# Kernel optimization log

Hardware: AMD Instinct MI355X
Metric: run time of the kernel (lower is better)

Reference implementation:

```python
import jax, jax.numpy as jnp
import numpy as np

H = 32        # num query heads
KVH = 8       # num kv heads
HD = 64       # head dim
G = H // KVH  # GQA group size
THETA = 10000.0


def _rope(x, pos):
    # x: [B, h, S, HD], pos: [B, S] int
    inv_freq = 1.0 / (THETA ** (jnp.arange(0, HD, 2, dtype=jnp.float32) / HD))  # [HD/2]
    freqs = pos.astype(jnp.float32)[:, :, None] * inv_freq[None, None, :]        # [B, S, HD/2]
    emb = jnp.concatenate([freqs, freqs], axis=-1)                               # [B, S, HD]
    cos = jnp.cos(emb)[:, None, :, :].astype(x.dtype)                            # [B, 1, S, HD]
    sin = jnp.sin(emb)[:, None, :, :].astype(x.dtype)
    x1, x2 = x[..., : HD // 2], x[..., HD // 2 :]
    rot = jnp.concatenate([-x2, x1], axis=-1)
    return x * cos + rot * sin


def setup_inputs() -> dict:
    key = jax.random.key(0)
    ks = jax.random.split(key, 8)
    B, S, D = 2, 2048, 2048
    s = 0.02
    hidden_states = jax.random.normal(ks[0], (B, S, D), dtype=jnp.float32)
    position_ids = jnp.broadcast_to(jnp.arange(S, dtype=jnp.int32)[None, :], (B, S))
    Wq = jax.random.normal(ks[1], (H * HD, D), dtype=jnp.float32) * s
    bq = jax.random.normal(ks[2], (H * HD,), dtype=jnp.float32) * s
    Wk = jax.random.normal(ks[3], (KVH * HD, D), dtype=jnp.float32) * s
    bk = jax.random.normal(ks[4], (KVH * HD,), dtype=jnp.float32) * s
    Wv = jax.random.normal(ks[5], (KVH * HD, D), dtype=jnp.float32) * s
    bv = jax.random.normal(ks[6], (KVH * HD,), dtype=jnp.float32) * s
    Wo = jax.random.normal(ks[7], (D, H * HD), dtype=jnp.float32) * s
    return dict(hidden_states=hidden_states, position_ids=position_ids,
                Wq=Wq, bq=bq, Wk=Wk, bk=bk, Wv=Wv, bv=bv, Wo=Wo)


def reference(hidden_states, position_ids, Wq, bq, Wk, bk, Wv, bv, Wo):
    B, S, D = hidden_states.shape
    scale = 1.0 / np.sqrt(HD)
    q = hidden_states @ Wq.T + bq  # [B, S, H*HD]
    k = hidden_states @ Wk.T + bk  # [B, S, KVH*HD]
    v = hidden_states @ Wv.T + bv
    q = q.reshape(B, S, H, HD).transpose(0, 2, 1, 3)      # [B, H, S, HD]
    k = k.reshape(B, S, KVH, HD).transpose(0, 2, 1, 3)    # [B, KVH, S, HD]
    v = v.reshape(B, S, KVH, HD).transpose(0, 2, 1, 3)
    q = _rope(q, position_ids)
    k = _rope(k, position_ids)
    # GQA: view q as [B, KVH, G, S, HD]; equivalent math to repeat_kv of k/v
    qg = q.reshape(B, KVH, G, S, HD)
    scores = jnp.einsum('bkgqd,bkld->bkgql', qg, k) * scale  # [B, KVH, G, S, S]
    # causal mask (past_seq_len = 0)
    causal = jnp.tril(jnp.ones((S, S), dtype=bool))
    scores = jnp.where(causal[None, None, None, :, :], scores, jnp.float32(-jnp.inf))
    attn = jax.nn.softmax(scores.astype(jnp.float32), axis=-1).astype(q.dtype)
    out = jnp.einsum('bkgql,bkld->bkgqd', attn, v)            # [B, KVH, G, S, HD]
    out = out.reshape(B, H, S, HD).transpose(0, 2, 1, 3).reshape(B, S, H * HD)
    return out @ Wo.T
```

## Files before the change

kernel.cpp:

```cpp
#include <hip/hip_runtime.h>
#include <hip/hip_bf16.h>

typedef unsigned short u16;
typedef __bf16 bf16x8 __attribute__((ext_vector_type(8)));
typedef float f32x4 __attribute__((ext_vector_type(4)));
typedef float f32x4v __attribute__((ext_vector_type(4)));
typedef unsigned short u16x4 __attribute__((ext_vector_type(4)));

__device__ __forceinline__ u16 f2bf(float f) {
  __bf16 h = (__bf16)f;
  return __builtin_bit_cast(unsigned short, h);
}

__device__ __forceinline__ int permh(int ph) {
  int blk = ph >> 4;
  int pblk = (blk == 1) ? 2 : ((blk == 2) ? 1 : blk);
  return (pblk << 4) | (ph & 15);
}

__device__ __forceinline__ int SW(int r, int c) {
  return (r << 6) + (c ^ ((r & 7) << 3));
}

#define GLOAD_LDS16(gp, lp) __builtin_amdgcn_global_load_lds( \
    (const __attribute__((address_space(1))) unsigned int*)(gp), \
    (__attribute__((address_space(3))) unsigned int*)(lp), 16, 0, 0)

#define BAR() do { asm volatile("" ::: "memory"); __builtin_amdgcn_s_barrier(); asm volatile("" ::: "memory"); } while (0)
#define VMCNT(n) asm volatile("s_waitcnt vmcnt(" #n ")" ::: "memory")
#define SBAR0() __builtin_amdgcn_sched_barrier(0)

__global__ void prep_all(const f32x4v* __restrict__ hs, u16x4* __restrict__ hsb,
                         const f32x4v* __restrict__ wq, const f32x4v* __restrict__ wk,
                         const f32x4v* __restrict__ wv, u16x4* __restrict__ wqkvb,
                         const f32x4v* __restrict__ wo, u16x4* __restrict__ wob,
                         const int* __restrict__ pos, float* __restrict__ cosT,
                         float* __restrict__ sinT, const float* __restrict__ bq,
                         const float* __restrict__ bk, const float* __restrict__ bv,
                         float* __restrict__ bc) {
  int i = blockIdx.x * 256 + threadIdx.x;
  if (i < 2097152) {
    f32x4v v = hs[i];
    u16x4 o; o.x = f2bf(v.x); o.y = f2bf(v.y); o.z = f2bf(v.z); o.w = f2bf(v.w);
    hsb[i] = o;
  } else if (i < 3670016) {
    int j = i - 2097152;
    int row = j >> 9, c4 = j & 511;
    f32x4v v;
    if (row < 2048) {
      int sr = (row & ~63) | permh(row & 63);
      v = wq[(size_t)sr * 512 + c4];
    } else if (row < 2560) {
      int rk = row - 2048;
      int sr = (rk & ~63) | permh(rk & 63);
      v = wk[(size_t)sr * 512 + c4];
    } else {
      v = wv[(size_t)(row - 2560) * 512 + c4];
    }
    u16x4 o; o.x = f2bf(v.x); o.y = f2bf(v.y); o.z = f2bf(v.z); o.w = f2bf(v.w);
    wqkvb[j] = o;
  } else if (i < 4718592) {
    int j = i - 3670016;
    f32x4v v = wo[j];
    u16x4 o; o.x = f2bf(v.x); o.y = f2bf(v.y); o.z = f2bf(v.z); o.w = f2bf(v.w);
    wob[j] = o;
  } else if (i < 4849664) {
    int j = i - 4718592;
    int bs = j >> 5, f = j & 31;
    float inv = exp2f(-(float)f * (13.287712379549449f / 32.f));
    float ang = (float)pos[bs] * inv;
    cosT[j] = cosf(ang);
    sinT[j] = sinf(ang);
  } else if (i < 4852736) {
    int j = i - 4849664;
    float v;
    if (j < 2048) {
      v = bq[(j & ~63) | permh(j & 63)];
    } else if (j < 2560) {
      int jk = j - 2048;
      v = bk[(jk & ~63) | permh(jk & 63)];
    } else {
      v = bv[j - 2560];
    }
    bc[j] = v;
  }
}

#define STAGE_A(kt, hh) { \
    const u16* s_ = aS + (size_t)(hh) * (BM / 2) * K + (size_t)(kt) * 64; \
    u16* d_ = lds + ((kt) & 1) * BUF + (hh) * (BM * 32) + wid * 512; \
    GLOAD_LDS16(s_, d_); \
    if constexpr (BM == 256) GLOAD_LDS16(s_ + (size_t)64 * K, d_ + 4096); \
  }

#define STAGE_B(kt, hh) { \
    const u16* s_ = bS + (size_t)(hh) * 128 * K + (size_t)(kt) * 64; \
    u16* d_ = lds + ((kt) & 1) * BUF + BM * 64 + (hh) * 8192 + wid * 512; \
    GLOAD_LDS16(s_, d_); \
    GLOAD_LDS16(s_ + (size_t)64 * K, d_ + 4096); \
  }

#define LDA8(buf, qm) { \
    const u16* p_ = lds + (buf) * BUF + ((qm) * (BM / 2) + arow) * 64; \
    _Pragma("unroll") \
    for (int mf = 0; mf < MF; ++mf) { \
      af[mf][0] = *(const bf16x8*)(p_ + mf * 1024 + koff0); \
      af[mf][1] = *(const bf16x8*)(p_ + mf * 1024 + koff1); \
    } }

#define LDB8(buf, qn) { \
    const u16* p_ = lds + (buf) * BUF + BM * 64 + ((qn) * 128 + brow) * 64; \
    _Pragma("unroll") \
    for (int nf = 0; nf < 2; ++nf) { \
      bfr[nf][0] = *(const bf16x8*)(p_ + nf * 1024 + koff0); \
      bfr[nf][1] = *(const bf16x8*)(p_ + nf * 1024 + koff1); \
    } }

#define MM8(qm, qn) { \
    __builtin_amdgcn_s_setprio(1); \
    _Pragma("unroll") \
    for (int mf = 0; mf < MF; ++mf) \
      _Pragma("unroll") \
      for (int nf = 0; nf < 2; ++nf) { \
        acc[(qm) * MF + mf][(qn) * 2 + nf] = __builtin_amdgcn_mfma_f32_16x16x32_bf16( \
            af[mf][0], bfr[nf][0], acc[(qm) * MF + mf][(qn) * 2 + nf], 0, 0, 0); \
        acc[(qm) * MF + mf][(qn) * 2 + nf] = __builtin_amdgcn_mfma_f32_16x16x32_bf16( \
            af[mf][1], bfr[nf][1], acc[(qm) * MF + mf][(qn) * 2 + nf], 0, 0, 0); \
      } \
    __builtin_amdgcn_s_setprio(0); }

#define VMCNT_GATE() do { if constexpr (BM == 256) { VMCNT(6); } else { VMCNT(4); } } while (0)

template <int MODE, int BM>
__global__ __launch_bounds__(512, 2) void gemm8(
    const u16* __restrict__ A, const u16* __restrict__ Bw, const int K, const int N,
    u16* __restrict__ qb, u16* __restrict__ kb, u16* __restrict__ vtb,
    const float* __restrict__ biasc, const float* __restrict__ cosT,
    const float* __restrict__ sinT, float* __restrict__ outf) {
  constexpr int MF = BM / 64;
  constexpr int BUF = BM * 64 + 16384;
  __shared__ u16 lds[2 * BUF];
  const int tid = threadIdx.x;
  const int lane = tid & 63, wid = tid >> 6;
  const int wr = wid >> 2, wc = wid & 3;
  const int col = lane & 15, rg = lane >> 4;
  const int tm = blockIdx.x, tn = blockIdx.y;

  const int srow = tid >> 3;
  const int scol = ((tid & 7) ^ (srow & 7)) * 8;
  const u16* aS = A + ((size_t)tm * BM + srow) * K + scol;
  const u16* bS = Bw + ((size_t)tn * 256 + srow) * K + scol;

  const int koff0 = (rg ^ (col & 7)) * 8;
  const int koff1 = ((4 + rg) ^ (col & 7)) * 8;
  const int arow = wr * (BM / 4) + col;
  const int brow = wc * 32 + col;

  f32x4 acc[2 * MF][4];
#pragma unroll
  for (int i = 0; i < 2 * MF; ++i)
#pragma unroll
    for (int j = 0; j < 4; ++j) acc[i][j] = (f32x4){0.f, 0.f, 0.f, 0.f};
  bf16x8 af[MF][2], bfr[2][2];

  const int ITERS = K >> 7;

  STAGE_A(0, 0); STAGE_A(0, 1);
  STAGE_B(0, 0); STAGE_B(0, 1);
  STAGE_A(1, 0); STAGE_B(1, 1); STAGE_A(1, 1);
  VMCNT_GATE();
  BAR();

#pragma unroll 1
  for (int it = 0; it < ITERS; ++it) {
    const int t0 = it * 2;
    const bool more = (it + 1 < ITERS);
    LDA8(0, 0); LDB8(0, 0);
    STAGE_B(t0 + 1, 0);
    MM8(0, 0); SBAR0(); BAR();
    LDB8(0, 1);
    if (more) STAGE_A(t0 + 2, 0);
    MM8(0, 1); SBAR0(); BAR();
    LDA8(0, 1);
    if (more) STAGE_B(t0 + 2, 1);
    MM8(1, 1); SBAR0(); BAR();
    LDB8(0, 0);
    if (more) STAGE_A(t0 + 2, 1);
    MM8(1, 0); SBAR0();
    if (more) { VMCNT_GATE(); } else { VMCNT(0); }
    BAR();
    LDA8(1, 0); LDB8(1, 0);
    if (more) STAGE_B(t0 + 2, 0);
    MM8(0, 0); SBAR0(); BAR();
    LDB8(1, 1);
    if (more) STAGE_A(t0 + 3, 0);
    MM8(0, 1); SBAR0(); BAR();
    LDA8(1, 1);
    if (more) STAGE_B(t0 + 3, 1);
    MM8(1, 1); SBAR0(); BAR();
    LDB8(1, 0);
    if (more) STAGE_A(t0 + 3, 1);
    MM8(1, 0); SBAR0();
    if (more) VMCNT_GATE();
    BAR();
  }

  if constexpr (MODE == 1) {
#pragma unroll
    for (int qm = 0; qm < 2; ++qm)
#pragma unroll
      for (int mf = 0; mf < MF; ++mf) {
        const int mbase = tm * BM + qm * (BM / 2) + wr * (BM / 4) + mf * 16 + rg * 4;
#pragma unroll
        for (int qn = 0; qn < 2; ++qn)
#pragma unroll
          for (int nf = 0; nf < 2; ++nf) {
            const int n = tn * 256 + qn * 128 + wc * 32 + nf * 16 + col;
#pragma unroll
            for (int r = 0; r < 4; ++r)
              outf[(size_t)(mbase + r) * N + n] = acc[qm * MF + mf][qn * 2 + nf][r];
          }
      }
  } else {
    if (tn < 8) {
      const float QS = 0.18033688011112042f;
#pragma unroll
      for (int qm = 0; qm < 2; ++qm)
#pragma unroll
        for (int qn = 0; qn < 2; ++qn) {
          const int h = tn * 4 + qn * 2 + (wc >> 1);
          const int c32 = wc & 1;
          const int n0 = tn * 256 + qn * 128 + wc * 32 + col;
          const float b1 = biasc[n0], b2 = biasc[n0 + 16];
          const int f = c32 * 16 + col;
          const int ph0 = c32 * 32 + col;
#pragma unroll
          for (int mf = 0; mf < MF; ++mf)
#pragma unroll
            for (int r = 0; r < 4; ++r) {
              const int m = tm * 256 + qm * 128 + wr * 64 + mf * 16 + rg * 4 + r;
              const int b = m >> 11, s = m & 2047;
              const size_t base = ((size_t)(b * 32 + h) * 2048 + s) * 64;
              float x1 = acc[qm * MF + mf][qn * 2 + 0][r] + b1;
              float x2 = acc[qm * MF + mf][qn * 2 + 1][r] + b2;
              float c = cosT[m * 32 + f], sn = sinT[m * 32 + f];
              qb[base + ph0]      = f2bf((x1 * c - x2 * sn) * QS);
              qb[base + ph0 + 16] = f2bf((x2 * c + x1 * sn) * QS);
            }
        }
    } else if (tn < 10) {
#pragma unroll
      for (int qm = 0; qm < 2; ++qm)
#pragma unroll
        for (int qn = 0; qn < 2; ++qn) {
          const int hk = (tn - 8) * 4 + qn * 2 + (wc >> 1);
          const int c32 = wc & 1;
          const int n0 = tn * 256 + qn * 128 + wc * 32 + col;
          const float b1 = biasc[n0], b2 = biasc[n0 + 16];
          const int f = c32 * 16 + col;
          const int ph0 = c32 * 32 + col;
#pragma unroll
          for (int mf = 0; mf < MF; ++mf)
#pragma unroll
            for (int r = 0; r < 4; ++r) {
              const int m = tm * 256 + qm * 128 + wr * 64 + mf * 16 + rg * 4 + r;
              const int b = m >> 11, s = m & 2047;
              const size_t base = ((size_t)(b * 8 + hk) * 2048 + s) * 64;
              float x1 = acc[qm * MF + mf][qn * 2 + 0][r] + b1;
              float x2 = acc[qm * MF + mf][qn * 2 + 1][r] + b2;
              float c = cosT[m * 32 + f], sn = sinT[m * 32 + f];
              kb[base + ph0]      = f2bf(x1 * c - x2 * sn);
              kb[base + ph0 + 16] = f2bf(x2 * c + x1 * sn);
            }
        }
    } else {
#pragma unroll
      for (int qm = 0; qm < 2; ++qm)
#pragma unroll
        for (int qn = 0; qn < 2; ++qn)
#pragma unroll
          for (int nf = 0; nf < 2; ++nf) {
            const int n = tn * 256 + qn * 128 + wc * 32 + nf * 16 + col;
            const int hk = (n - 2560) >> 6;
            const int d = (n - 2560) & 63;
            const float bvv = biasc[n];
#pragma unroll
            for (int mf = 0; mf < MF; ++mf)
#pragma unroll
              for (int r = 0; r < 4; ++r) {
                const int m = tm * 256 + qm * 128 + wr * 64 + mf * 16 + rg * 4 + r;
                const int b = m >> 11, s = m & 2047;
                vtb[((size_t)(b * 8 + hk) * 64 + d) * 2048 + s] =
                    f2bf(acc[qm * MF + mf][qn * 2 + nf][r] + bvv);
              }
          }
    }
  }
}

__global__ __launch_bounds__(256, 4) void attn_k(
    const u16* __restrict__ qb, const u16* __restrict__ kb,
    const u16* __restrict__ vtb, u16* __restrict__ attb) {
  __shared__ __align__(16) u16 Kl[3][2048];
  __shared__ __align__(16) u16 Vl[3][2048];
  __shared__ __align__(16) u16 Pl[4096];
  const int tid = threadIdx.x, lane = tid & 63, w = tid >> 6;
  const int col = lane & 15, rg = lane >> 4;

  const int bid = blockIdx.x;
  const int xcd = bid & 7, pos = bid >> 3;
  const int grp = xcd * 8 + (pos >> 4);
  const int s0 = pos & 15;
  const int strip = ((pos >> 5) & 1) ? (15 - s0) : s0;
  const int h = grp & 31, b = grp >> 5;
  const int qb0 = (15 - strip) * 128;
  const int hk = h >> 2;
  const int q0w = qb0 + w * 32;

  const u16* Qp = qb + ((size_t)(b * 32 + h) * 2048 + q0w + col) * 64 + rg * 8;
  bf16x8 qf[2][2];
#pragma unroll
  for (int g = 0; g < 2; ++g)
#pragma unroll
    for (int kf = 0; kf < 2; ++kf)
      qf[g][kf] = *(const bf16x8*)(Qp + g * 16 * 64 + kf * 32);

  f32x4 po[2][4];
  float l_part[2] = {0.f, 0.f};
#pragma unroll
  for (int g = 0; g < 2; ++g)
#pragma unroll
    for (int cf = 0; cf < 4; ++cf) po[g][cf] = (f32x4){0, 0, 0, 0};

  const u16* Kbase = kb + (size_t)(b * 8 + hk) * 2048 * 64;
  const u16* Vbase = vtb + (size_t)(b * 8 + hk) * 64 * 2048;
  const int srow = tid >> 3, c8 = (tid & 7) << 3;
  const int cs = c8 ^ ((srow & 7) << 3);
  const u16* Ksrc = Kbase + (size_t)srow * 64 + cs;
  const u16* Vsrc = Vbase + (size_t)(srow * 2 + (cs >> 5)) * 2048 + (cs & 31);
  char* Kdst0 = (char*)Kl + w * 1024;
  char* Vdst0 = (char*)Vl + w * 1024;

  const int nkv = (qb0 >> 5) + 4;
  const int rowmax = q0w + 31;

  GLOAD_LDS16(Ksrc, Kdst0);
  GLOAD_LDS16(Vsrc, Vdst0);
  GLOAD_LDS16(Ksrc + 2048, Kdst0 + 4096);
  GLOAD_LDS16(Vsrc + 32, Vdst0 + 4096);

  for (int it = 0; it < nkv; ++it) {
    const int kv0 = it * 32;
    const int buf = it % 3;
    if (it + 2 < nkv) {
      const int b2 = (it + 2) % 3;
      GLOAD_LDS16(Ksrc + (size_t)(it + 2) * 2048, Kdst0 + b2 * 4096);
      GLOAD_LDS16(Vsrc + (size_t)(it + 2) * 32, Vdst0 + b2 * 4096);
      VMCNT(4);
    } else if (it + 1 < nkv) {
      VMCNT(2);
    } else {
      VMCNT(0);
    }
    BAR();

    if (kv0 <= rowmax) {
      const u16* Kb = (const u16*)((const char*)Kl + buf * 4096);
      const u16* Vb = (const u16*)((const char*)Vl + buf * 4096);
      const bool diag = (kv0 + 32 > q0w);

#pragma unroll
      for (int cj = 0; cj < 2; ++cj) {
        const int krow = cj * 16 + col;
        bf16x8 k0f = *(const bf16x8*)&Kb[SW(krow, rg * 8)];
        bf16x8 k1f = *(const bf16x8*)&Kb[SW(krow, 32 + rg * 8)];
#pragma unroll
        for (int g = 0; g < 2; ++g) {
          f32x4 t = (f32x4){0, 0, 0, 0};
          t = __builtin_amdgcn_mfma_f32_16x16x32_bf16(k0f, qf[g][0], t, 0, 0, 0);
          t = __builtin_amdgcn_mfma_f32_16x16x32_bf16(k1f, qf[g][1], t, 0, 0, 0);
          const int q = q0w + g * 16 + col;
          if (diag) {
            const int kbase = kv0 + cj * 16 + rg * 4;
#pragma unroll
            for (int r = 0; r < 4; ++r)
              if (kbase + r > q) t[r] = -1e30f;
          }
          float p0 = __builtin_amdgcn_exp2f(t[0]);
          float p1 = __builtin_amdgcn_exp2f(t[1]);
          float p2 = __builtin_amdgcn_exp2f(t[2]);
          float p3 = __builtin_amdgcn_exp2f(t[3]);
          l_part[g] += (p0 + p1) + (p2 + p3);
          unsigned w0, w1;
          asm("v_cvt_pk_bf16_f32 %0, %1, %2" : "=v"(w0) : "v"(p0), "v"(p1));
          asm("v_cvt_pk_bf16_f32 %0, %1, %2" : "=v"(w1) : "v"(p2), "v"(p3));
          const int lq = w * 32 + g * 16 + col;
          const int prow = lq >> 1;
          const int pc = ((lq & 1) * 32 + cj * 16 + rg * 4) ^ ((prow & 7) << 3);
          *(uint2*)&Pl[prow * 64 + pc] = (uint2){w0, w1};
        }
      }

      __builtin_amdgcn_s_setprio(1);
      {
        bf16x8 pfr[2];
#pragma unroll
        for (int g = 0; g < 2; ++g) {
          const int lq = w * 32 + g * 16 + col;
          const int prow = lq >> 1;
          pfr[g] = *(const bf16x8*)&Pl[prow * 64 +
                     (((lq & 1) * 32 + rg * 8) ^ ((prow & 7) << 3))];
        }
#pragma unroll
        for (int cf = 0; cf < 4; ++cf) {
          const int d = cf * 16 + col;
          const int vrow = d >> 1;
          bf16x8 vf = *(const bf16x8*)&Vb[vrow * 64 +
                       (((d & 1) * 32 + rg * 8) ^ ((vrow & 7) << 3))];
          po[0][cf] = __builtin_amdgcn_mfma_f32_16x16x32_bf16(pfr[0], vf, po[0][cf], 0, 0, 0);
          po[1][cf] = __builtin_amdgcn_mfma_f32_16x16x32_bf16(pfr[1], vf, po[1][cf], 0, 0, 0);
        }
      }
      __builtin_amdgcn_s_setprio(0);
    }
    SBAR0();
    BAR();
  }

#pragma unroll
  for (int g = 0; g < 2; ++g) {
    float l = l_part[g];
    l += __shfl_xor(l, 16);
    l += __shfl_xor(l, 32);
    l_part[g] = l;
  }
#pragma unroll
  for (int g = 0; g < 2; ++g)
#pragma unroll
    for (int r = 0; r < 4; ++r) {
      const float lq = __shfl(l_part[g], rg * 4 + r, 16);
      const float inv = 1.f / lq;
      const int qrow = q0w + g * 16 + rg * 4 + r;
      size_t base = ((size_t)b * 2048 + qrow) * 2048 + h * 64;
#pragma unroll
      for (int cf = 0; cf < 4; ++cf)
        attb[base + cf * 16 + col] = f2bf(po[g][cf][r] * inv);
    }
}

extern "C" void kernel_launch(void* const* d_in, const int* in_sizes, int n_in,
                              void* d_out, int out_size, void* d_ws, size_t ws_size,
                              hipStream_t stream) {
  const float* hs = (const float*)d_in[0];
  const int* pos = (const int*)d_in[1];
  const float* Wq = (const float*)d_in[2];
  const float* bq = (const float*)d_in[3];
  const float* Wk = (const float*)d_in[4];
  const float* bk = (const float*)d_in[5];
  const float* Wv = (const float*)d_in[6];
  const float* bv = (const float*)d_in[7];
  const float* Wo = (const float*)d_in[8];
  float* out = (float*)d_out;

  char* ws = (char*)d_ws;
  size_t off = 0;
  u16* hsb = (u16*)(ws + off);   off += (size_t)4096 * 2048 * 2;
  u16* wqkvb = (u16*)(ws + off); off += (size_t)3072 * 2048 * 2;
  u16* wob = (u16*)(ws + off);   off += (size_t)2048 * 2048 * 2;
  float* biasc = (float*)(ws + off); off += 3072 * 4;
  float* cosT = (float*)(ws + off);  off += (size_t)4096 * 32 * 4;
  float* sinT = (float*)(ws + off);  off += (size_t)4096 * 32 * 4;
  u16* qb = (u16*)(ws + off);    off += (size_t)2 * 32 * 2048 * 64 * 2;
  u16* kb = (u16*)(ws + off);    off += (size_t)2 * 8 * 2048 * 64 * 2;
  u16* vtb = (u16*)(ws + off);   off += (size_t)2 * 8 * 64 * 2048 * 2;
  u16* attb = (u16*)(ws + off);  off += (size_t)4096 * 2048 * 2;

  prep_all<<<18956, 256, 0, stream>>>((const f32x4v*)hs, (u16x4*)hsb,
                                      (const f32x4v*)Wq, (const f32x4v*)Wk,
                                      (const f32x4v*)Wv, (u16x4*)wqkvb,
                                      (const f32x4v*)Wo, (u16x4*)wob,
                                      pos, cosT, sinT, bq, bk, bv, biasc);

  gemm8<0, 256><<<dim3(16, 12), 512, 0, stream>>>(hsb, wqkvb, 2048, 3072,
                                                  qb, kb, vtb, biasc, cosT, sinT, nullptr);
  attn_k<<<1024, 256, 0, stream>>>(qb, kb, vtb, attb);
  gemm8<1, 128><<<dim3(32, 8), 512, 0, stream>>>(attb, wob, 2048, 2048,
                                                 nullptr, nullptr, nullptr, nullptr,
                                                 nullptr, nullptr, out);
}
```

Measured before the change: 174.3 us.

## Double-buffer GEMM LDS fragments in registers to prefetch ahead of MFMA

The GEMM main loop now keeps two register sets each for the A and B fragments. The LDS reads for the next MFMA phase are issued before the current phase's MFMAs, so LDS latency overlaps with matrix math. The first fragments are loaded in the prologue and the last phase prefetches the next iteration's data. The vmcnt wait thresholds move to match the reordered staging. The extra fragment registers add VGPR pressure under the 512x2 launch bounds and could cause spills or lower occupancy.

```diff
diff --git a/kernel.cpp b/kernel.cpp
--- a/kernel.cpp
+++ b/kernel.cpp
@@ -100,36 +100,37 @@
     GLOAD_LDS16(s_ + (size_t)64 * K, d_ + 4096); \
   }
 
-#define LDA8(buf, qm) { \
+#define LDA8_TO(dst, buf, qm) { \
     const u16* p_ = lds + (buf) * BUF + ((qm) * (BM / 2) + arow) * 64; \
     _Pragma("unroll") \
     for (int mf = 0; mf < MF; ++mf) { \
-      af[mf][0] = *(const bf16x8*)(p_ + mf * 1024 + koff0); \
-      af[mf][1] = *(const bf16x8*)(p_ + mf * 1024 + koff1); \
+      dst[mf][0] = *(const bf16x8*)(p_ + mf * 1024 + koff0); \
+      dst[mf][1] = *(const bf16x8*)(p_ + mf * 1024 + koff1); \
     } }
 
-#define LDB8(buf, qn) { \
+#define LDB8_TO(dst, buf, qn) { \
     const u16* p_ = lds + (buf) * BUF + BM * 64 + ((qn) * 128 + brow) * 64; \
     _Pragma("unroll") \
     for (int nf = 0; nf < 2; ++nf) { \
-      bfr[nf][0] = *(const bf16x8*)(p_ + nf * 1024 + koff0); \
-      bfr[nf][1] = *(const bf16x8*)(p_ + nf * 1024 + koff1); \
+      dst[nf][0] = *(const bf16x8*)(p_ + nf * 1024 + koff0); \
+      dst[nf][1] = *(const bf16x8*)(p_ + nf * 1024 + koff1); \
     } }
 
-#define MM8(qm, qn) { \
+#define MM8_W(afs, bfs, qm, qn) { \
     __builtin_amdgcn_s_setprio(1); \
     _Pragma("unroll") \
     for (int mf = 0; mf < MF; ++mf) \
       _Pragma("unroll") \
       for (int nf = 0; nf < 2; ++nf) { \
         acc[(qm) * MF + mf][(qn) * 2 + nf] = __builtin_amdgcn_mfma_f32_16x16x32_bf16( \
-            af[mf][0], bfr[nf][0], acc[(qm) * MF + mf][(qn) * 2 + nf], 0, 0, 0); \
+            afs[mf][0], bfs[nf][0], acc[(qm) * MF + mf][(qn) * 2 + nf], 0, 0, 0); \
         acc[(qm) * MF + mf][(qn) * 2 + nf] = __builtin_amdgcn_mfma_f32_16x16x32_bf16( \
-            af[mf][1], bfr[nf][1], acc[(qm) * MF + mf][(qn) * 2 + nf], 0, 0, 0); \
+            afs[mf][1], bfs[nf][1], acc[(qm) * MF + mf][(qn) * 2 + nf], 0, 0, 0); \
       } \
     __builtin_amdgcn_s_setprio(0); }
 
-#define VMCNT_GATE() do { if constexpr (BM == 256) { VMCNT(6); } else { VMCNT(4); } } while (0)
+#define VM_G() do { if constexpr (BM == 256) { VMCNT(4); } else { VMCNT(3); } } while (0)
+#define VM_PRO() do { if constexpr (BM == 256) { VMCNT(6); } else { VMCNT(4); } } while (0)
 
 template <int MODE, int BM>
 __global__ __launch_bounds__(512, 2) void gemm8(
@@ -161,48 +162,51 @@
   for (int i = 0; i < 2 * MF; ++i)
 #pragma unroll
     for (int j = 0; j < 4; ++j) acc[i][j] = (f32x4){0.f, 0.f, 0.f, 0.f};
-  bf16x8 af[MF][2], bfr[2][2];
+  bf16x8 afX[MF][2], afY[MF][2], bfA[2][2], bfB[2][2];
 
   const int ITERS = K >> 7;
 
   STAGE_A(0, 0); STAGE_A(0, 1);
   STAGE_B(0, 0); STAGE_B(0, 1);
   STAGE_A(1, 0); STAGE_B(1, 1); STAGE_A(1, 1);
-  VMCNT_GATE();
+  VM_PRO();
   BAR();
+  LDA8_TO(afX, 0, 0); LDB8_TO(bfA, 0, 0);
 
 #pragma unroll 1
   for (int it = 0; it < ITERS; ++it) {
     const int t0 = it * 2;
     const bool more = (it + 1 < ITERS);
-    LDA8(0, 0); LDB8(0, 0);
     STAGE_B(t0 + 1, 0);
-    MM8(0, 0); SBAR0(); BAR();
-    LDB8(0, 1);
+    LDB8_TO(bfB, 0, 1);
+    SBAR0(); MM8_W(afX, bfA, 0, 0); SBAR0(); BAR();
     if (more) STAGE_A(t0 + 2, 0);
-    MM8(0, 1); SBAR0(); BAR();
-    LDA8(0, 1);
+    LDA8_TO(afY, 0, 1);
+    SBAR0(); MM8_W(afX, bfB, 0, 1); SBAR0(); BAR();
     if (more) STAGE_B(t0 + 2, 1);
-    MM8(1, 1); SBAR0(); BAR();
-    LDB8(0, 0);
+    LDB8_TO(bfA, 0, 0);
+    SBAR0(); MM8_W(afY, bfB, 1, 1); SBAR0();
+    if (more) { VM_G(); } else { VMCNT(0); }
+    BAR();
     if (more) STAGE_A(t0 + 2, 1);
-    MM8(1, 0); SBAR0();
-    if (more) { VMCNT_GATE(); } else { VMCNT(0); }
+    LDA8_TO(afX, 1, 0); LDB8_TO(bfB, 1, 0);
+    SBAR0(); MM8_W(afY, bfA, 1, 0); SBAR0(); BAR();
+    if (more) STAGE_B(t0 + 2, 0);
+    LDB8_TO(bfA, 1, 1);
+    SBAR0(); MM8_W(afX, bfB, 0, 0); SBAR0(); BAR();
+    if (more) STAGE_A(t0 + 3, 0);
+    LDA8_TO(afY, 1, 1);
+    SBAR0(); MM8_W(afX, bfA, 0, 1); SBAR0(); BAR();
+    if (more) STAGE_B(t0 + 3, 1);
+    LDB8_TO(bfB, 1, 0);
+    SBAR0(); MM8_W(afY, bfA, 1, 1); SBAR0();
+    if (more) VM_G();
     BAR();
-    LDA8(1, 0); LDB8(1, 0);
-    if (more) STAGE_B(t0 + 2, 0);
-    MM8(0, 0); SBAR0(); BAR();
-    LDB8(1, 1);
-    if (more) STAGE_A(t0 + 3, 0);
-    MM8(0, 1); SBAR0(); BAR();
-    LDA8(1, 1);
-    if (more) STAGE_B(t0 + 3, 1);
-    MM8(1, 1); SBAR0(); BAR();
-    LDB8(1, 0);
-    if (more) STAGE_A(t0 + 3, 1);
-    MM8(1, 0); SBAR0();
-    if (more) VMCNT_GATE();
-    BAR();
+    if (more) {
+      STAGE_A(t0 + 3, 1);
+      LDA8_TO(afX, 0, 0); LDB8_TO(bfA, 0, 0);
+    }
+    SBAR0(); MM8_W(afY, bfB, 1, 0); SBAR0(); BAR();
   }
 
   if constexpr (MODE == 1) {
```

Measured after the change: 207.9 us. +19.3%, slower.

## Switch attention to 32x32x16 MFMA and keep P in registers via permlane swap

Applied to the files above, without the earlier changes.

The attention kernel now computes each wave's 32x32 score tile with 32x32x16 bf16 MFMAs instead of 16x16x32 tiles. The exp'd probabilities are packed to bf16 and rearranged across lanes with v_permlane32_swap, so they feed the PV MFMA straight from registers. This drops the LDS round-trip for P and its shared buffer, and the row-sum reduction and output store are simplified to match the new layout. The cost is higher register pressure from the 16-wide accumulators, and the cross-lane layout must be exactly right for the result to be correct.

```diff
diff --git a/kernel.cpp b/kernel.cpp
--- a/kernel.cpp
+++ b/kernel.cpp
@@ -4,12 +4,21 @@
 typedef unsigned short u16;
 typedef __bf16 bf16x8 __attribute__((ext_vector_type(8)));
 typedef float f32x4 __attribute__((ext_vector_type(4)));
+typedef float f32x16 __attribute__((ext_vector_type(16)));
 typedef float f32x4v __attribute__((ext_vector_type(4)));
 typedef unsigned short u16x4 __attribute__((ext_vector_type(4)));
+typedef unsigned int u32x4 __attribute__((ext_vector_type(4)));
 
 __device__ __forceinline__ u16 f2bf(float f) {
   __bf16 h = (__bf16)f;
   return __builtin_bit_cast(unsigned short, h);
+}
+
+__device__ __forceinline__ f32x16 z16() {
+  f32x16 z;
+#pragma unroll
+  for (int i = 0; i < 16; ++i) z[i] = 0.f;
+  return z;
 }
 
 __device__ __forceinline__ int permh(int ph) {
@@ -303,9 +312,8 @@
     const u16* __restrict__ vtb, u16* __restrict__ attb) {
   __shared__ __align__(16) u16 Kl[3][2048];
   __shared__ __align__(16) u16 Vl[3][2048];
-  __shared__ __align__(16) u16 Pl[4096];
   const int tid = threadIdx.x, lane = tid & 63, w = tid >> 6;
-  const int col = lane & 15, rg = lane >> 4;
+  const int q32 = lane & 31, hl = lane >> 5, h4 = hl * 4;
 
   const int bid = blockIdx.x;
   const int xcd = bid & 7, pos = bid >> 3;
@@ -317,20 +325,14 @@
   const int hk = h >> 2;
   const int q0w = qb0 + w * 32;
 
-  const u16* Qp = qb + ((size_t)(b * 32 + h) * 2048 + q0w + col) * 64 + rg * 8;
-  bf16x8 qf[2][2];
-#pragma unroll
-  for (int g = 0; g < 2; ++g)
-#pragma unroll
-    for (int kf = 0; kf < 2; ++kf)
-      qf[g][kf] = *(const bf16x8*)(Qp + g * 16 * 64 + kf * 32);
-
-  f32x4 po[2][4];
-  float l_part[2] = {0.f, 0.f};
-#pragma unroll
-  for (int g = 0; g < 2; ++g)
-#pragma unroll
-    for (int cf = 0; cf < 4; ++cf) po[g][cf] = (f32x4){0, 0, 0, 0};
+  const u16* Qp = qb + ((size_t)(b * 32 + h) * 2048 + q0w + q32) * 64 + hl * 8;
+  bf16x8 qf[4];
+#pragma unroll
+  for (int s = 0; s < 4; ++s) qf[s] = *(const bf16x8*)(Qp + s * 16);
+
+  f32x16 po[2];
+  po[0] = z16(); po[1] = z16();
+  float l_part = 0.f;
 
   const u16* Kbase = kb + (size_t)(b * 8 + hk) * 2048 * 64;
   const u16* Vbase = vtb + (size_t)(b * 8 + hk) * 64 * 2048;
@@ -369,57 +371,50 @@
       const u16* Vb = (const u16*)((const char*)Vl + buf * 4096);
       const bool diag = (kv0 + 32 > q0w);
 
-#pragma unroll
-      for (int cj = 0; cj < 2; ++cj) {
-        const int krow = cj * 16 + col;
-        bf16x8 k0f = *(const bf16x8*)&Kb[SW(krow, rg * 8)];
-        bf16x8 k1f = *(const bf16x8*)&Kb[SW(krow, 32 + rg * 8)];
-#pragma unroll
-        for (int g = 0; g < 2; ++g) {
-          f32x4 t = (f32x4){0, 0, 0, 0};
-          t = __builtin_amdgcn_mfma_f32_16x16x32_bf16(k0f, qf[g][0], t, 0, 0, 0);
-          t = __builtin_amdgcn_mfma_f32_16x16x32_bf16(k1f, qf[g][1], t, 0, 0, 0);
-          const int q = q0w + g * 16 + col;
-          if (diag) {
-            const int kbase = kv0 + cj * 16 + rg * 4;
-#pragma unroll
-            for (int r = 0; r < 4; ++r)
-              if (kbase + r > q) t[r] = -1e30f;
-          }
-          float p0 = __builtin_amdgcn_exp2f(t[0]);
-          float p1 = __builtin_amdgcn_exp2f(t[1]);
-          float p2 = __builtin_amdgcn_exp2f(t[2]);
-          float p3 = __builtin_amdgcn_exp2f(t[3]);
-          l_part[g] += (p0 + p1) + (p2 + p3);
-          unsigned w0, w1;
-          asm("v_cvt_pk_bf16_f32 %0, %1, %2" : "=v"(w0) : "v"(p0), "v"(p1));
-          asm("v_cvt_pk_bf16_f32 %0, %1, %2" : "=v"(w1) : "v"(p2), "v"(p3));
-          const int lq = w * 32 + g * 16 + col;
-          const int prow = lq >> 1;
-          const int pc = ((lq & 1) * 32 + cj * 16 + rg * 4) ^ ((prow & 7) << 3);
-          *(uint2*)&Pl[prow * 64 + pc] = (uint2){w0, w1};
+      f32x16 t = z16();
+#pragma unroll
+      for (int s = 0; s < 4; ++s) {
+        bf16x8 kf = *(const bf16x8*)&Kb[SW(q32, s * 16 + hl * 8)];
+        t = __builtin_amdgcn_mfma_f32_32x32x16_bf16(kf, qf[s], t, 0, 0, 0);
+      }
+      if (diag) {
+        const int qg = q0w + q32;
+#pragma unroll
+        for (int r = 0; r < 16; ++r) {
+          const int kvg = kv0 + (r & 3) + 8 * (r >> 2) + h4;
+          if (kvg > qg) t[r] = -1e30f;
         }
       }
+#pragma unroll
+      for (int r = 0; r < 16; ++r) t[r] = __builtin_amdgcn_exp2f(t[r]);
+      l_part += (((t[0] + t[1]) + (t[2] + t[3])) + ((t[4] + t[5]) + (t[6] + t[7]))) +
+                (((t[8] + t[9]) + (t[10] + t[11])) + ((t[12] + t[13]) + (t[14] + t[15])));
+
+      unsigned pw0, pw1, pw2, pw3, pw4, pw5, pw6, pw7;
+      asm("v_cvt_pk_bf16_f32 %0, %1, %2" : "=v"(pw0) : "v"(t[0]), "v"(t[1]));
+      asm("v_cvt_pk_bf16_f32 %0, %1, %2" : "=v"(pw1) : "v"(t[2]), "v"(t[3]));
+      asm("v_cvt_pk_bf16_f32 %0, %1, %2" : "=v"(pw2) : "v"(t[4]), "v"(t[5]));
+      asm("v_cvt_pk_bf16_f32 %0, %1, %2" : "=v"(pw3) : "v"(t[6]), "v"(t[7]));
+      asm("v_cvt_pk_bf16_f32 %0, %1, %2" : "=v"(pw4) : "v"(t[8]), "v"(t[9]));
+      asm("v_cvt_pk_bf16_f32 %0, %1, %2" : "=v"(pw5) : "v"(t[10]), "v"(t[11]));
+      asm("v_cvt_pk_bf16_f32 %0, %1, %2" : "=v"(pw6) : "v"(t[12]), "v"(t[13]));
+      asm("v_cvt_pk_bf16_f32 %0, %1, %2" : "=v"(pw7) : "v"(t[14]), "v"(t[15]));
+      asm("v_permlane32_swap_b32 %0, %1" : "+v"(pw0), "+v"(pw2));
+      asm("v_permlane32_swap_b32 %0, %1" : "+v"(pw1), "+v"(pw3));
+      asm("v_permlane32_swap_b32 %0, %1" : "+v"(pw4), "+v"(pw6));
+      asm("v_permlane32_swap_b32 %0, %1" : "+v"(pw5), "+v"(pw7));
+      const bf16x8 pa0 = __builtin_bit_cast(bf16x8, (u32x4){pw0, pw1, pw2, pw3});
+      const bf16x8 pa1 = __builtin_bit_cast(bf16x8, (u32x4){pw4, pw5, pw6, pw7});
 
       __builtin_amdgcn_s_setprio(1);
-      {
-        bf16x8 pfr[2];
-#pragma unroll
-        for (int g = 0; g < 2; ++g) {
-          const int lq = w * 32 + g * 16 + col;
-          const int prow = lq >> 1;
-          pfr[g] = *(const bf16x8*)&Pl[prow * 64 +
-                     (((lq & 1) * 32 + rg * 8) ^ ((prow & 7) << 3))];
-        }
-#pragma unroll
-        for (int cf = 0; cf < 4; ++cf) {
-          const int d = cf * 16 + col;
-          const int vrow = d >> 1;
-          bf16x8 vf = *(const bf16x8*)&Vb[vrow * 64 +
-                       (((d & 1) * 32 + rg * 8) ^ ((vrow & 7) << 3))];
-          po[0][cf] = __builtin_amdgcn_mfma_f32_16x16x32_bf16(pfr[0], vf, po[0][cf], 0, 0, 0);
-          po[1][cf] = __builtin_amdgcn_mfma_f32_16x16x32_bf16(pfr[1], vf, po[1][cf], 0, 0, 0);
-        }
+#pragma unroll
+      for (int dblk = 0; dblk < 2; ++dblk) {
+        const int d = dblk * 32 + q32;
+        const int vr = d >> 1, vc = (d & 1) * 32 + hl * 8;
+        bf16x8 v0 = *(const bf16x8*)&Vb[SW(vr, vc)];
+        bf16x8 v1 = *(const bf16x8*)&Vb[SW(vr, vc + 16)];
+        po[dblk] = __builtin_amdgcn_mfma_f32_32x32x16_bf16(pa0, v0, po[dblk], 0, 0, 0);
+        po[dblk] = __builtin_amdgcn_mfma_f32_32x32x16_bf16(pa1, v1, po[dblk], 0, 0, 0);
       }
       __builtin_amdgcn_s_setprio(0);
     }
@@ -427,25 +422,16 @@
     BAR();
   }
 
-#pragma unroll
-  for (int g = 0; g < 2; ++g) {
-    float l = l_part[g];
-    l += __shfl_xor(l, 16);
-    l += __shfl_xor(l, 32);
-    l_part[g] = l;
-  }
-#pragma unroll
-  for (int g = 0; g < 2; ++g)
-#pragma unroll
-    for (int r = 0; r < 4; ++r) {
-      const float lq = __shfl(l_part[g], rg * 4 + r, 16);
-      const float inv = 1.f / lq;
-      const int qrow = q0w + g * 16 + rg * 4 + r;
-      size_t base = ((size_t)b * 2048 + qrow) * 2048 + h * 64;
-#pragma unroll
-      for (int cf = 0; cf < 4; ++cf)
-        attb[base + cf * 16 + col] = f2bf(po[g][cf][r] * inv);
-    }
+  const float l_full = l_part + __shfl_xor(l_part, 32);
+#pragma unroll
+  for (int r = 0; r < 16; ++r) {
+    const int qrl = (r & 3) + 8 * (r >> 2) + h4;
+    const float lq = __shfl(l_full, qrl);
+    const float inv = 1.f / lq;
+    const size_t base = ((size_t)b * 2048 + q0w + qrl) * 2048 + h * 64;
+    attb[base + q32]      = f2bf(po[0][r] * inv);
+    attb[base + 32 + q32] = f2bf(po[1][r] * inv);
+  }
 }
 
 extern "C" void kernel_launch(void* const* d_in, const int* in_sizes, int n_in,
```

New measurement: 172.5 us. No clear change (-1.0%).
